# Kernel tuning notes

Measured on AMD Instinct MI355X. Metric: run time of the kernel, lower is better.

The kernel has to match this reference:

```python
import jax, jax.numpy as jnp
import numpy as np

B, F, N = 16, 128, 20000  # batch, feature (edge==node==message size), num nodes
M = F  # message_size = edge_feature_size


def setup_inputs() -> dict:
    key = jax.random.key(0)
    ks = jax.random.split(key, 9)
    s = 1.0 / np.sqrt(F)
    return {
        "h_w": jax.random.normal(ks[0], (B, F, N), jnp.float32),
        "h_v": jax.random.normal(ks[1], (B, F), jnp.float32),
        "e_wv": jax.random.normal(ks[2], (B, F, N), jnp.float32),
        "W_e2m": jax.random.normal(ks[3], (M, F), jnp.float32) * s,
        "b_e2m": jax.random.normal(ks[4], (M,), jnp.float32) * s,
        "W_n2m": jax.random.normal(ks[5], (M, F), jnp.float32) * s,
        "b_n2m": jax.random.normal(ks[6], (M,), jnp.float32) * s,
        "W_resize": jax.random.normal(ks[7], (M, 3 * M), jnp.float32) * (1.0 / np.sqrt(3 * M)),
        "b_resize": jax.random.normal(ks[8], (M,), jnp.float32) * (1.0 / np.sqrt(3 * M)),
    }


def reference(h_w, h_v, e_wv, W_e2m, b_e2m, W_n2m, b_n2m, W_resize, b_resize):
    # Per-node loop vectorized over the node axis n.
    # tmp_msg = cat([e2m(e_wv[:,:,n]), n2m(h_w[:,:,n]), n2m(h_v)], dim=1)
    # message[:,:,n] = resize_m(tmp_msg)
    # Split W_resize into its three column blocks to avoid materializing the
    # [B, 3M, N] concat: resize(cat(a,b,c)) = Wa@a + Wb@b + Wc@c + b.
    Wa = W_resize[:, :M]          # acts on e2m output
    Wb = W_resize[:, M:2 * M]     # acts on n2m(h_w)
    Wc = W_resize[:, 2 * M:]      # acts on n2m(h_v)

    em = jnp.einsum('bfn,mf->bmn', e_wv, W_e2m) + b_e2m[:, None]   # [B,M,N]
    nw = jnp.einsum('bfn,mf->bmn', h_w, W_n2m) + b_n2m[:, None]    # [B,M,N]
    nv = h_v @ W_n2m.T + b_n2m                                      # [B,M]

    msg = (jnp.einsum('bmn,km->bkn', em, Wa)
           + jnp.einsum('bmn,km->bkn', nw, Wb)
           + ((nv @ Wc.T) + b_resize)[:, :, None])                  # [B,M,N]
    return msg
```

## Files before the change

### kernel.cpp

```cpp
#include <hip/hip_runtime.h>
#include <hip/hip_bf16.h>

typedef __attribute__((ext_vector_type(8))) short bf16x8;
typedef __attribute__((ext_vector_type(4))) float f32x4;

#define F_DIM 128
#define N_DIM 20000
#define M_DIM 128
#define NW 32
#define TILES_PER_B 625
#define NT 20
#define GRID 500
#define F32_TILE 32768
#define F32_MAT 16384
#define BF16_OFF 65536
#define BF16_MAT 8192

#define AS1 __attribute__((address_space(1)))
#define AS3 __attribute__((address_space(3)))

static __device__ inline unsigned short f2bf(float x) {
    union { float f; unsigned u; } v; v.f = x;
    unsigned r = v.u + 0x7fffu + ((v.u >> 16) & 1u);
    return (unsigned short)(r >> 16);
}

__global__ __launch_bounds__(256) void precompute_mats(
    const float* __restrict__ W_rs,
    const float* __restrict__ W_e2m,
    const float* __restrict__ W_n2m,
    unsigned short* __restrict__ wsA,
    unsigned short* __restrict__ wsB)
{
    int idx = blockIdx.x * 256 + threadIdx.x;
    int k = idx >> 7;
    int f = idx & 127;
    float a = 0.f, b = 0.f;
    for (int m = 0; m < 128; ++m) {
        a += W_rs[k * 384 + m]       * W_e2m[m * 128 + f];
        b += W_rs[k * 384 + 128 + m] * W_n2m[m * 128 + f];
    }
    int mt = k >> 4, row = k & 15;
    int c = f >> 5, kk = f & 31;
    int lane = ((kk >> 3) << 4) | row;
    int j = kk & 7;
    int off = ((mt * 4 + c) * 64 + lane) * 8 + j;
    wsA[off] = f2bf(a);
    wsB[off] = f2bf(b);
}

__global__ __launch_bounds__(128) void precompute_bias(
    const float* __restrict__ W_rs,
    const float* __restrict__ h_v,
    const float* __restrict__ b_e2m,
    const float* __restrict__ b_n2m,
    const float* __restrict__ b_rs,
    const float* __restrict__ W_n2m,
    float* __restrict__ bias)
{
    __shared__ float nv_s[128];
    int b = blockIdx.x;
    int t = threadIdx.x;
    {
        float nv = b_n2m[t];
        for (int f = 0; f < 128; ++f)
            nv += h_v[b * 128 + f] * W_n2m[t * 128 + f];
        nv_s[t] = nv;
    }
    __syncthreads();
    {
        float acc = b_rs[t];
        for (int m = 0; m < 128; ++m) {
            acc += W_rs[t * 384 + m]       * b_e2m[m];
            acc += W_rs[t * 384 + 128 + m] * b_n2m[m];
            acc += W_rs[t * 384 + 256 + m] * nv_s[m];
        }
        bias[b * 128 + t] = acc;
    }
}

__global__ __launch_bounds__(256, 2) void msg_main(
    const float* __restrict__ e_wv,
    const float* __restrict__ h_w,
    const unsigned short* __restrict__ wsA,
    const unsigned short* __restrict__ wsB,
    const float* __restrict__ bias,
    float* __restrict__ out)
{
    __shared__ __align__(16) unsigned char smem[81920];

    int tid = threadIdx.x;
    int w   = tid >> 6;
    int l   = tid & 63;
    unsigned base = (unsigned)blockIdx.x * NT;

    const bf16x8* Af = (const bf16x8*)wsA;
    const bf16x8* Bf = (const bf16x8*)wsB;
    bf16x8 A0[4], A1[4], B0[4], B1[4];
#pragma unroll
    for (int c = 0; c < 4; ++c) {
        A0[c] = Af[((2 * w + 0) * 4 + c) * 64 + l];
        A1[c] = Af[((2 * w + 1) * 4 + c) * 64 + l];
        B0[c] = Bf[((2 * w + 0) * 4 + c) * 64 + l];
        B1[c] = Bf[((2 * w + 1) * 4 + c) * 64 + l];
    }

    int fl = l >> 3, p = l & 7;
    auto issue_dma = [&](unsigned tau, unsigned bufsel) {
        unsigned bb = tau / TILES_PER_B;
        unsigned n0 = (tau - bb * TILES_PER_B) * NW;
        const float* eb = e_wv + (size_t)bb * (F_DIM * (size_t)N_DIM) + n0;
        const float* wp = h_w  + (size_t)bb * (F_DIM * (size_t)N_DIM) + n0;
        unsigned char* buf = smem + bufsel * F32_TILE;
#pragma unroll
        for (int i = 0; i < 4; ++i) {
            int fb = i * 32 + w * 8;
            int f  = fb + fl;
            int g  = (f ^ (f >> 3)) & 7;
            int col = (p ^ g) << 2;
            __builtin_amdgcn_global_load_lds(
                (const AS1 unsigned*)(eb + (size_t)f * N_DIM + col),
                (AS3 unsigned*)(buf + fb * 128), 16, 0, 0);
            __builtin_amdgcn_global_load_lds(
                (const AS1 unsigned*)(wp + (size_t)f * N_DIM + col),
                (AS3 unsigned*)(buf + F32_MAT + fb * 128), 16, 0, 0);
        }
    };

    auto transform = [&](unsigned bufsel) {
        const unsigned char* fsrc = smem + bufsel * F32_TILE + (tid >> 7) * F32_MAT;
        unsigned char* bdst = smem + BF16_OFF + (tid >> 7) * BF16_MAT;
        int u = tid & 127;
        int fp = u >> 1, half = u & 1;
        int f0 = 2 * fp, f1 = 2 * fp + 1;
        int g0 = (f0 ^ (f0 >> 3)) & 7, g1 = (f1 ^ (f1 >> 3)) & 7;
#pragma unroll
        for (int j = 0; j < 4; ++j) {
            int q = half * 4 + j;
            f32x4 a = *(const f32x4*)(fsrc + f0 * 128 + ((q ^ g0) << 4));
            f32x4 c = *(const f32x4*)(fsrc + f1 * 128 + ((q ^ g1) << 4));
#pragma unroll
            for (int e = 0; e < 4; ++e) {
                int n = q * 4 + e;
                unsigned pk = (unsigned)f2bf(a[e]) | ((unsigned)f2bf(c[e]) << 16);
                unsigned off = (unsigned)(n * 256) +
                               (((unsigned)(fp * 4)) ^ ((unsigned)((n & 7) << 4)));
                *(unsigned*)(bdst + off) = pk;
            }
        }
    };

    issue_dma(base + 0, 0);
    issue_dma(base + 1, 1);
    asm volatile("s_waitcnt vmcnt(8)" ::: "memory");
    __builtin_amdgcn_s_barrier();
    transform(0);
    asm volatile("s_waitcnt lgkmcnt(0)" ::: "memory");
    __builtin_amdgcn_s_barrier();

    int ln = l & 15, g = l >> 4;
    unsigned rbase = (unsigned)(ln * 256);
    unsigned rx = (unsigned)((ln & 7) << 4);
    const unsigned char* ldse = smem + BF16_OFF;
    const unsigned char* ldsw = smem + BF16_OFF + BF16_MAT;

#pragma unroll 1
    for (int t = 0; t < NT; ++t) {
        unsigned tau = base + t;
        unsigned bb = tau / TILES_PER_B;
        unsigned n0 = (tau - bb * TILES_PER_B) * NW;

        const float* bp = bias + bb * 128;
        f32x4 bv0 = *(const f32x4*)(bp + (2 * w + 0) * 16 + g * 4);
        f32x4 bv1 = *(const f32x4*)(bp + (2 * w + 1) * 16 + g * 4);

        int t2 = t + 2; if (t2 >= NT) t2 -= NT;
        issue_dma(base + t2, (unsigned)(t & 1));

        f32x4 acc[2][2];
#pragma unroll
        for (int mtL = 0; mtL < 2; ++mtL)
#pragma unroll
            for (int ns = 0; ns < 2; ++ns) acc[mtL][ns] = (f32x4)(0.f);
#pragma unroll
        for (int c = 0; c < 4; ++c) {
            unsigned fbyte = (unsigned)((c * 32 + g * 8) * 2) ^ rx;
#pragma unroll
            for (int ns = 0; ns < 2; ++ns) {
                bf16x8 xe = *(const bf16x8*)(ldse + ns * 4096 + rbase + fbyte);
                bf16x8 xw = *(const bf16x8*)(ldsw + ns * 4096 + rbase + fbyte);
                acc[0][ns] = __builtin_amdgcn_mfma_f32_16x16x32_bf16(A0[c], xe, acc[0][ns], 0, 0, 0);
                acc[0][ns] = __builtin_amdgcn_mfma_f32_16x16x32_bf16(B0[c], xw, acc[0][ns], 0, 0, 0);
                acc[1][ns] = __builtin_amdgcn_mfma_f32_16x16x32_bf16(A1[c], xe, acc[1][ns], 0, 0, 0);
                acc[1][ns] = __builtin_amdgcn_mfma_f32_16x16x32_bf16(B1[c], xw, acc[1][ns], 0, 0, 0);
            }
        }

        asm volatile("s_waitcnt vmcnt(8)" ::: "memory");
        asm volatile("s_waitcnt lgkmcnt(0)" ::: "memory");
        __builtin_amdgcn_s_barrier();

        if (t < NT - 1) transform((unsigned)((t + 1) & 1));
        asm volatile("s_waitcnt lgkmcnt(0)" ::: "memory");
        __builtin_amdgcn_s_barrier();

        float* O = out + (size_t)bb * (M_DIM * (size_t)N_DIM) + n0 + ln;
#pragma unroll
        for (int mtL = 0; mtL < 2; ++mtL) {
            f32x4 bv = mtL ? bv1 : bv0;
            int mt = 2 * w + mtL;
#pragma unroll
            for (int ns = 0; ns < 2; ++ns)
#pragma unroll
                for (int r = 0; r < 4; ++r)
                    O[(size_t)(mt * 16 + g * 4 + r) * N_DIM + ns * 16] =
                        acc[mtL][ns][r] + bv[r];
        }
    }

    asm volatile("s_waitcnt vmcnt(0)" ::: "memory");
}

extern "C" void kernel_launch(void* const* d_in, const int* in_sizes, int n_in,
                              void* d_out, int out_size, void* d_ws, size_t ws_size,
                              hipStream_t stream) {
    const float* h_w   = (const float*)d_in[0];
    const float* h_v   = (const float*)d_in[1];
    const float* e_wv  = (const float*)d_in[2];
    const float* W_e2m = (const float*)d_in[3];
    const float* b_e2m = (const float*)d_in[4];
    const float* W_n2m = (const float*)d_in[5];
    const float* b_n2m = (const float*)d_in[6];
    const float* W_rs  = (const float*)d_in[7];
    const float* b_rs  = (const float*)d_in[8];
    float* out = (float*)d_out;

    unsigned short* wsA = (unsigned short*)d_ws;
    unsigned short* wsB = wsA + 128 * 128;
    float* bias = (float*)((char*)d_ws + 65536);

    precompute_mats<<<64, 256, 0, stream>>>(W_rs, W_e2m, W_n2m, wsA, wsB);
    precompute_bias<<<16, 128, 0, stream>>>(W_rs, h_v, b_e2m, b_n2m, b_rs, W_n2m, bias);
    msg_main<<<GRID, 256, 0, stream>>>(e_wv, h_w, wsA, wsB, bias, out);
}
```

Measured before the change: 134.4 us.

## Replace LDS DMA staging with register prefetch and direct bf16 LDS writes

Drops the global_load_lds fp32 staging buffer and the separate LDS-to-LDS transform pass. Each thread now prefetches the next tile's fp32 inputs into registers, converts them with the packed v_cvt_pk_bf16_f32 instruction, and writes bf16 straight into a double-buffered LDS tile after the current tile's MFMAs and stores. Grid grows from 500 to 1250 blocks with 8 tiles each, LDS shrinks to 32 KB, and the launch-bounds occupancy hint is removed. The cost is higher register pressure from the prefetch registers and only one tile of lookahead instead of two.

New measurement: 191.8 us. +42.7%, slower.

```diff
diff --git a/kernel.cpp b/kernel.cpp
--- a/kernel.cpp
+++ b/kernel.cpp
@@ -9,20 +9,21 @@
 #define M_DIM 128
 #define NW 32
 #define TILES_PER_B 625
-#define NT 20
-#define GRID 500
-#define F32_TILE 32768
-#define F32_MAT 16384
-#define BF16_OFF 65536
-#define BF16_MAT 8192
-
-#define AS1 __attribute__((address_space(1)))
-#define AS3 __attribute__((address_space(3)))
+#define NT 8
+#define GRID 1250
+#define BUF_STRIDE 16384
+#define MAT_STRIDE 8192
 
 static __device__ inline unsigned short f2bf(float x) {
     union { float f; unsigned u; } v; v.f = x;
     unsigned r = v.u + 0x7fffu + ((v.u >> 16) & 1u);
     return (unsigned short)(r >> 16);
+}
+
+static __device__ inline unsigned cvt_pk_bf16(float lo, float hi) {
+    unsigned r;
+    asm("v_cvt_pk_bf16_f32 %0, %1, %2" : "=v"(r) : "v"(lo), "v"(hi));
+    return r;
 }
 
 __global__ __launch_bounds__(256) void precompute_mats(
@@ -79,7 +80,7 @@
     }
 }
 
-__global__ __launch_bounds__(256, 2) void msg_main(
+__global__ void msg_main(
     const float* __restrict__ e_wv,
     const float* __restrict__ h_w,
     const unsigned short* __restrict__ wsA,
@@ -87,7 +88,7 @@
     const float* __restrict__ bias,
     float* __restrict__ out)
 {
-    __shared__ __align__(16) unsigned char smem[81920];
+    __shared__ __align__(16) unsigned char smem[2 * BUF_STRIDE];
 
     int tid = threadIdx.x;
     int w   = tid >> 6;
@@ -105,64 +106,48 @@
         B1[c] = Bf[((2 * w + 1) * 4 + c) * 64 + l];
     }
 
-    int fl = l >> 3, p = l & 7;
-    auto issue_dma = [&](unsigned tau, unsigned bufsel) {
+    int r = l >> 3;
+    int q = l & 7;
+
+    f32x4 ve[2][2], vw[2][2];
+    auto load_tile = [&](unsigned tau) {
         unsigned bb = tau / TILES_PER_B;
         unsigned n0 = (tau - bb * TILES_PER_B) * NW;
-        const float* eb = e_wv + (size_t)bb * (F_DIM * (size_t)N_DIM) + n0;
-        const float* wp = h_w  + (size_t)bb * (F_DIM * (size_t)N_DIM) + n0;
-        unsigned char* buf = smem + bufsel * F32_TILE;
-#pragma unroll
-        for (int i = 0; i < 4; ++i) {
-            int fb = i * 32 + w * 8;
-            int f  = fb + fl;
-            int g  = (f ^ (f >> 3)) & 7;
-            int col = (p ^ g) << 2;
-            __builtin_amdgcn_global_load_lds(
-                (const AS1 unsigned*)(eb + (size_t)f * N_DIM + col),
-                (AS3 unsigned*)(buf + fb * 128), 16, 0, 0);
-            __builtin_amdgcn_global_load_lds(
-                (const AS1 unsigned*)(wp + (size_t)f * N_DIM + col),
-                (AS3 unsigned*)(buf + F32_MAT + fb * 128), 16, 0, 0);
-        }
+        const float* eb = e_wv + (size_t)bb * (F_DIM * (size_t)N_DIM) + n0 + 4 * q;
+        const float* wb = h_w  + (size_t)bb * (F_DIM * (size_t)N_DIM) + n0 + 4 * q;
+#pragma unroll
+        for (int j = 0; j < 2; ++j)
+#pragma unroll
+            for (int par = 0; par < 2; ++par) {
+                int f = w * 32 + j * 16 + 2 * r + par;
+                ve[j][par] = *(const f32x4*)(eb + (size_t)f * N_DIM);
+                vw[j][par] = *(const f32x4*)(wb + (size_t)f * N_DIM);
+            }
     };
 
-    auto transform = [&](unsigned bufsel) {
-        const unsigned char* fsrc = smem + bufsel * F32_TILE + (tid >> 7) * F32_MAT;
-        unsigned char* bdst = smem + BF16_OFF + (tid >> 7) * BF16_MAT;
-        int u = tid & 127;
-        int fp = u >> 1, half = u & 1;
-        int f0 = 2 * fp, f1 = 2 * fp + 1;
-        int g0 = (f0 ^ (f0 >> 3)) & 7, g1 = (f1 ^ (f1 >> 3)) & 7;
-#pragma unroll
-        for (int j = 0; j < 4; ++j) {
-            int q = half * 4 + j;
-            f32x4 a = *(const f32x4*)(fsrc + f0 * 128 + ((q ^ g0) << 4));
-            f32x4 c = *(const f32x4*)(fsrc + f1 * 128 + ((q ^ g1) << 4));
+    auto cvt_write = [&](unsigned bufsel) {
+        unsigned char* be = smem + bufsel * BUF_STRIDE;
+        unsigned char* bw = be + MAT_STRIDE;
+#pragma unroll
+        for (int j = 0; j < 2; ++j) {
+            unsigned fp = (unsigned)(w * 16 + j * 8 + r);
 #pragma unroll
             for (int e = 0; e < 4; ++e) {
-                int n = q * 4 + e;
-                unsigned pk = (unsigned)f2bf(a[e]) | ((unsigned)f2bf(c[e]) << 16);
-                unsigned off = (unsigned)(n * 256) +
-                               (((unsigned)(fp * 4)) ^ ((unsigned)((n & 7) << 4)));
-                *(unsigned*)(bdst + off) = pk;
+                unsigned nn = (unsigned)(4 * q + e);
+                unsigned off = nn * 256 + ((fp * 4) ^ ((nn & 7) << 4));
+                *(unsigned*)(be + off) = cvt_pk_bf16(ve[j][0][e], ve[j][1][e]);
+                *(unsigned*)(bw + off) = cvt_pk_bf16(vw[j][0][e], vw[j][1][e]);
             }
         }
     };
 
-    issue_dma(base + 0, 0);
-    issue_dma(base + 1, 1);
-    asm volatile("s_waitcnt vmcnt(8)" ::: "memory");
-    __builtin_amdgcn_s_barrier();
-    transform(0);
-    asm volatile("s_waitcnt lgkmcnt(0)" ::: "memory");
-    __builtin_amdgcn_s_barrier();
+    load_tile(base);
+    cvt_write(0);
+    __syncthreads();
 
     int ln = l & 15, g = l >> 4;
     unsigned rbase = (unsigned)(ln * 256);
     unsigned rx = (unsigned)((ln & 7) << 4);
-    const unsigned char* ldse = smem + BF16_OFF;
-    const unsigned char* ldsw = smem + BF16_OFF + BF16_MAT;
 
 #pragma unroll 1
     for (int t = 0; t < NT; ++t) {
@@ -174,9 +159,10 @@
         f32x4 bv0 = *(const f32x4*)(bp + (2 * w + 0) * 16 + g * 4);
         f32x4 bv1 = *(const f32x4*)(bp + (2 * w + 1) * 16 + g * 4);
 
-        int t2 = t + 2; if (t2 >= NT) t2 -= NT;
-        issue_dma(base + t2, (unsigned)(t & 1));
-
+        if (t + 1 < NT) load_tile(base + t + 1);
+        __builtin_amdgcn_sched_barrier(0);
+
+        const unsigned char* bufp = smem + (unsigned)(t & 1) * BUF_STRIDE;
         f32x4 acc[2][2];
 #pragma unroll
         for (int mtL = 0; mtL < 2; ++mtL)
@@ -187,8 +173,8 @@
             unsigned fbyte = (unsigned)((c * 32 + g * 8) * 2) ^ rx;
 #pragma unroll
             for (int ns = 0; ns < 2; ++ns) {
-                bf16x8 xe = *(const bf16x8*)(ldse + ns * 4096 + rbase + fbyte);
-                bf16x8 xw = *(const bf16x8*)(ldsw + ns * 4096 + rbase + fbyte);
+                bf16x8 xe = *(const bf16x8*)(bufp + ns * 4096 + rbase + fbyte);
+                bf16x8 xw = *(const bf16x8*)(bufp + MAT_STRIDE + ns * 4096 + rbase + fbyte);
                 acc[0][ns] = __builtin_amdgcn_mfma_f32_16x16x32_bf16(A0[c], xe, acc[0][ns], 0, 0, 0);
                 acc[0][ns] = __builtin_amdgcn_mfma_f32_16x16x32_bf16(B0[c], xw, acc[0][ns], 0, 0, 0);
                 acc[1][ns] = __builtin_amdgcn_mfma_f32_16x16x32_bf16(A1[c], xe, acc[1][ns], 0, 0, 0);
@@ -196,14 +182,6 @@
             }
         }
 
-        asm volatile("s_waitcnt vmcnt(8)" ::: "memory");
-        asm volatile("s_waitcnt lgkmcnt(0)" ::: "memory");
-        __builtin_amdgcn_s_barrier();
-
-        if (t < NT - 1) transform((unsigned)((t + 1) & 1));
-        asm volatile("s_waitcnt lgkmcnt(0)" ::: "memory");
-        __builtin_amdgcn_s_barrier();
-
         float* O = out + (size_t)bb * (M_DIM * (size_t)N_DIM) + n0 + ln;
 #pragma unroll
         for (int mtL = 0; mtL < 2; ++mtL) {
@@ -212,13 +190,14 @@
 #pragma unroll
             for (int ns = 0; ns < 2; ++ns)
 #pragma unroll
-                for (int r = 0; r < 4; ++r)
-                    O[(size_t)(mt * 16 + g * 4 + r) * N_DIM + ns * 16] =
-                        acc[mtL][ns][r] + bv[r];
-        }
-    }
-
-    asm volatile("s_waitcnt vmcnt(0)" ::: "memory");
+                for (int rr = 0; rr < 4; ++rr)
+                    O[(size_t)(mt * 16 + g * 4 + rr) * N_DIM + ns * 16] =
+                        acc[mtL][ns][rr] + bv[rr];
+        }
+
+        if (t + 1 < NT) cvt_write((unsigned)((t + 1) & 1));
+        __syncthreads();
+    }
 }
 
 extern "C" void kernel_launch(void* const* d_in, const int* in_sizes, int n_in,
```

## Restructure main kernel to 512-thread blocks with triple-buffered paired DMA

Applied to the files above, without the earlier changes.

Doubles block size to 512 threads (one block per CU, 250 blocks, 40 tiles each), triple-buffers the fp32 staging in LDS and issues DMA for two tiles at a time every other iteration. Swaps MFMA operand order so each lane stores four contiguous outputs with a 16-byte vector store. Replaces the software bf16 rounding with the hardware v_cvt_pk_bf16_f32 instruction. The goal is deeper prefetch and fewer, wider global stores; the cost is lower occupancy, dummy loads at the tail, and hand-tuned vmcnt values that must stay exact.

Result: slower. 146.0 us (+8.6%).

```diff
diff --git a/kernel.cpp b/kernel.cpp
--- a/kernel.cpp
+++ b/kernel.cpp
@@ -9,11 +9,11 @@
 #define M_DIM 128
 #define NW 32
 #define TILES_PER_B 625
-#define NT 20
-#define GRID 500
-#define F32_TILE 32768
+#define NT 40
+#define GRID 250
+#define F32_BUF 32768
 #define F32_MAT 16384
-#define BF16_OFF 65536
+#define BF16_OFF 98304
 #define BF16_MAT 8192
 
 #define AS1 __attribute__((address_space(1)))
@@ -23,6 +23,12 @@
     union { float f; unsigned u; } v; v.f = x;
     unsigned r = v.u + 0x7fffu + ((v.u >> 16) & 1u);
     return (unsigned short)(r >> 16);
+}
+
+static __device__ inline unsigned cvt_pk_bf16(float lo, float hi) {
+    unsigned r;
+    asm("v_cvt_pk_bf16_f32 %0, %1, %2" : "=v"(r) : "v"(lo), "v"(hi));
+    return r;
 }
 
 __global__ __launch_bounds__(256) void precompute_mats(
@@ -79,7 +85,7 @@
     }
 }
 
-__global__ __launch_bounds__(256, 2) void msg_main(
+__global__ __launch_bounds__(512, 1) void msg_main(
     const float* __restrict__ e_wv,
     const float* __restrict__ h_w,
     const unsigned short* __restrict__ wsA,
@@ -87,7 +93,7 @@
     const float* __restrict__ bias,
     float* __restrict__ out)
 {
-    __shared__ __align__(16) unsigned char smem[81920];
+    __shared__ __align__(16) unsigned char smem[114688];
 
     int tid = threadIdx.x;
     int w   = tid >> 6;
@@ -96,53 +102,73 @@
 
     const bf16x8* Af = (const bf16x8*)wsA;
     const bf16x8* Bf = (const bf16x8*)wsB;
-    bf16x8 A0[4], A1[4], B0[4], B1[4];
+    bf16x8 A[4], B[4];
 #pragma unroll
     for (int c = 0; c < 4; ++c) {
-        A0[c] = Af[((2 * w + 0) * 4 + c) * 64 + l];
-        A1[c] = Af[((2 * w + 1) * 4 + c) * 64 + l];
-        B0[c] = Bf[((2 * w + 0) * 4 + c) * 64 + l];
-        B1[c] = Bf[((2 * w + 1) * 4 + c) * 64 + l];
+        A[c] = Af[(w * 4 + c) * 64 + l];
+        B[c] = Bf[(w * 4 + c) * 64 + l];
     }
 
     int fl = l >> 3, p = l & 7;
-    auto issue_dma = [&](unsigned tau, unsigned bufsel) {
+    int ln = l & 15, g = l >> 4;
+
+    auto dma_unit = [&](unsigned tau, unsigned bufidx, int i) {
         unsigned bb = tau / TILES_PER_B;
         unsigned n0 = (tau - bb * TILES_PER_B) * NW;
-        const float* eb = e_wv + (size_t)bb * (F_DIM * (size_t)N_DIM) + n0;
-        const float* wp = h_w  + (size_t)bb * (F_DIM * (size_t)N_DIM) + n0;
-        unsigned char* buf = smem + bufsel * F32_TILE;
+        int unit = w * 4 + i;
+        int mat = unit >> 4;
+        int rg  = unit & 15;
+        int f   = rg * 8 + fl;
+        int gx  = (f ^ (f >> 3)) & 7;
+        int col = (p ^ gx) << 2;
+        const float* src = (mat ? h_w : e_wv)
+            + (size_t)bb * (F_DIM * (size_t)N_DIM) + n0 + (size_t)f * N_DIM + col;
+        unsigned char* dst = smem + bufidx * F32_BUF + mat * F32_MAT + rg * 1024;
+        __builtin_amdgcn_global_load_lds((const AS1 unsigned*)src,
+                                         (AS3 unsigned*)dst, 16, 0, 0);
+    };
+
+    auto issue_pair = [&](unsigned tauA, unsigned bufA, unsigned tauB, unsigned bufB) {
 #pragma unroll
         for (int i = 0; i < 4; ++i) {
-            int fb = i * 32 + w * 8;
-            int f  = fb + fl;
-            int g  = (f ^ (f >> 3)) & 7;
-            int col = (p ^ g) << 2;
-            __builtin_amdgcn_global_load_lds(
-                (const AS1 unsigned*)(eb + (size_t)f * N_DIM + col),
-                (AS3 unsigned*)(buf + fb * 128), 16, 0, 0);
-            __builtin_amdgcn_global_load_lds(
-                (const AS1 unsigned*)(wp + (size_t)f * N_DIM + col),
-                (AS3 unsigned*)(buf + F32_MAT + fb * 128), 16, 0, 0);
-        }
-    };
-
-    auto transform = [&](unsigned bufsel) {
-        const unsigned char* fsrc = smem + bufsel * F32_TILE + (tid >> 7) * F32_MAT;
-        unsigned char* bdst = smem + BF16_OFF + (tid >> 7) * BF16_MAT;
-        int u = tid & 127;
-        int fp = u >> 1, half = u & 1;
+            dma_unit(tauA, bufA, i);
+            dma_unit(tauB, bufB, i);
+        }
+    };
+
+    auto dummy_pair = [&](unsigned bufA, unsigned bufB) {
+#pragma unroll
+        for (int i = 0; i < 4; ++i) {
+            int unit = w * 4 + i;
+            int mat = unit >> 4;
+            int rg  = unit & 15;
+            unsigned char* dA = smem + bufA * F32_BUF + mat * F32_MAT + rg * 1024;
+            unsigned char* dB = smem + bufB * F32_BUF + mat * F32_MAT + rg * 1024;
+            __builtin_amdgcn_global_load_lds((const AS1 unsigned*)e_wv,
+                                             (AS3 unsigned*)dA, 16, 0, 0);
+            __builtin_amdgcn_global_load_lds((const AS1 unsigned*)h_w,
+                                             (AS3 unsigned*)dB, 16, 0, 0);
+        }
+    };
+
+    auto transform = [&](unsigned bufidx) {
+        int mat = tid >> 8;
+        int u   = tid & 255;
+        int fp  = u >> 2;
+        int qh  = u & 3;
+        const unsigned char* fsrc = smem + bufidx * F32_BUF + mat * F32_MAT;
+        unsigned char* bdst = smem + BF16_OFF + mat * BF16_MAT;
         int f0 = 2 * fp, f1 = 2 * fp + 1;
         int g0 = (f0 ^ (f0 >> 3)) & 7, g1 = (f1 ^ (f1 >> 3)) & 7;
 #pragma unroll
-        for (int j = 0; j < 4; ++j) {
-            int q = half * 4 + j;
+        for (int j = 0; j < 2; ++j) {
+            int q = qh * 2 + j;
             f32x4 a = *(const f32x4*)(fsrc + f0 * 128 + ((q ^ g0) << 4));
             f32x4 c = *(const f32x4*)(fsrc + f1 * 128 + ((q ^ g1) << 4));
 #pragma unroll
             for (int e = 0; e < 4; ++e) {
                 int n = q * 4 + e;
-                unsigned pk = (unsigned)f2bf(a[e]) | ((unsigned)f2bf(c[e]) << 16);
+                unsigned pk = cvt_pk_bf16(a[e], c[e]);
                 unsigned off = (unsigned)(n * 256) +
                                (((unsigned)(fp * 4)) ^ ((unsigned)((n & 7) << 4)));
                 *(unsigned*)(bdst + off) = pk;
@@ -150,15 +176,13 @@
         }
     };
 
-    issue_dma(base + 0, 0);
-    issue_dma(base + 1, 1);
-    asm volatile("s_waitcnt vmcnt(8)" ::: "memory");
+    issue_pair(base + 0, 0, base + 1, 1);
+    asm volatile("s_waitcnt vmcnt(1)" ::: "memory");
     __builtin_amdgcn_s_barrier();
     transform(0);
     asm volatile("s_waitcnt lgkmcnt(0)" ::: "memory");
     __builtin_amdgcn_s_barrier();
 
-    int ln = l & 15, g = l >> 4;
     unsigned rbase = (unsigned)(ln * 256);
     unsigned rx = (unsigned)((ln & 7) << 4);
     const unsigned char* ldse = smem + BF16_OFF;
@@ -170,18 +194,19 @@
         unsigned bb = tau / TILES_PER_B;
         unsigned n0 = (tau - bb * TILES_PER_B) * NW;
 
-        const float* bp = bias + bb * 128;
-        f32x4 bv0 = *(const f32x4*)(bp + (2 * w + 0) * 16 + g * 4);
-        f32x4 bv1 = *(const f32x4*)(bp + (2 * w + 1) * 16 + g * 4);
-
-        int t2 = t + 2; if (t2 >= NT) t2 -= NT;
-        issue_dma(base + t2, (unsigned)(t & 1));
-
-        f32x4 acc[2][2];
-#pragma unroll
-        for (int mtL = 0; mtL < 2; ++mtL)
-#pragma unroll
-            for (int ns = 0; ns < 2; ++ns) acc[mtL][ns] = (f32x4)(0.f);
+        float bvc = bias[bb * 128 + w * 16 + ln];
+
+        if ((t & 1) == 0) {
+            if (t + 3 < NT)
+                issue_pair(base + t + 2, (unsigned)((t + 2) % 3),
+                           base + t + 3, (unsigned)((t + 3) % 3));
+            else
+                dummy_pair((unsigned)((t + 2) % 3), (unsigned)((t + 3) % 3));
+        }
+
+        f32x4 acc[2];
+        acc[0] = (f32x4)(0.f);
+        acc[1] = (f32x4)(0.f);
 #pragma unroll
         for (int c = 0; c < 4; ++c) {
             unsigned fbyte = (unsigned)((c * 32 + g * 8) * 2) ^ rx;
@@ -189,32 +214,28 @@
             for (int ns = 0; ns < 2; ++ns) {
                 bf16x8 xe = *(const bf16x8*)(ldse + ns * 4096 + rbase + fbyte);
                 bf16x8 xw = *(const bf16x8*)(ldsw + ns * 4096 + rbase + fbyte);
-                acc[0][ns] = __builtin_amdgcn_mfma_f32_16x16x32_bf16(A0[c], xe, acc[0][ns], 0, 0, 0);
-                acc[0][ns] = __builtin_amdgcn_mfma_f32_16x16x32_bf16(B0[c], xw, acc[0][ns], 0, 0, 0);
-                acc[1][ns] = __builtin_amdgcn_mfma_f32_16x16x32_bf16(A1[c], xe, acc[1][ns], 0, 0, 0);
-                acc[1][ns] = __builtin_amdgcn_mfma_f32_16x16x32_bf16(B1[c], xw, acc[1][ns], 0, 0, 0);
+                acc[ns] = __builtin_amdgcn_mfma_f32_16x16x32_bf16(xe, A[c], acc[ns], 0, 0, 0);
+                acc[ns] = __builtin_amdgcn_mfma_f32_16x16x32_bf16(xw, B[c], acc[ns], 0, 0, 0);
             }
         }
 
-        asm volatile("s_waitcnt vmcnt(8)" ::: "memory");
+        if (t == 0)      { asm volatile("s_waitcnt vmcnt(9)"  ::: "memory"); }
+        else if (t & 1)  { asm volatile("s_waitcnt vmcnt(4)"  ::: "memory"); }
+        else             { asm volatile("s_waitcnt vmcnt(14)" ::: "memory"); }
         asm volatile("s_waitcnt lgkmcnt(0)" ::: "memory");
         __builtin_amdgcn_s_barrier();
 
-        if (t < NT - 1) transform((unsigned)((t + 1) & 1));
+        if (t < NT - 1) transform((unsigned)((t + 1) % 3));
         asm volatile("s_waitcnt lgkmcnt(0)" ::: "memory");
         __builtin_amdgcn_s_barrier();
 
-        float* O = out + (size_t)bb * (M_DIM * (size_t)N_DIM) + n0 + ln;
-#pragma unroll
-        for (int mtL = 0; mtL < 2; ++mtL) {
-            f32x4 bv = mtL ? bv1 : bv0;
-            int mt = 2 * w + mtL;
-#pragma unroll
-            for (int ns = 0; ns < 2; ++ns)
-#pragma unroll
-                for (int r = 0; r < 4; ++r)
-                    O[(size_t)(mt * 16 + g * 4 + r) * N_DIM + ns * 16] =
-                        acc[mtL][ns][r] + bv[r];
+        float* O = out + (size_t)bb * (M_DIM * (size_t)N_DIM) + n0;
+        int k = w * 16 + ln;
+#pragma unroll
+        for (int ns = 0; ns < 2; ++ns) {
+            f32x4 v = acc[ns];
+            v[0] += bvc; v[1] += bvc; v[2] += bvc; v[3] += bvc;
+            *(f32x4*)(O + (size_t)k * N_DIM + ns * 16 + g * 4) = v;
         }
     }
 
@@ -241,5 +262,5 @@
 
     precompute_mats<<<64, 256, 0, stream>>>(W_rs, W_e2m, W_n2m, wsA, wsB);
     precompute_bias<<<16, 128, 0, stream>>>(W_rs, h_v, b_e2m, b_n2m, b_rs, W_n2m, bias);
-    msg_main<<<GRID, 256, 0, stream>>>(e_wv, h_w, wsA, wsB, bias, out);
-}
+    msg_main<<<GRID, 512, 0, stream>>>(e_wv, h_w, wsA, wsB, bias, out);
+}
```
